# Kernel optimization log

Measured on AMD Instinct MI355X. Metric: run time of the kernel, lower is better.

## Reference

```python
import jax, jax.numpy as jnp
import numpy as np

EMBED_DIM = 1024
NUM_HEADS = 16
HEAD_DIM = EMBED_DIM // NUM_HEADS
VOCAB = 5          # languages
BOTTLENECK = 800
SCALING = HEAD_DIM ** -0.5


def setup_inputs() -> dict:
    key = jax.random.key(0)
    ks = jax.random.split(key, 16)
    T, B, D = 2048, 2, EMBED_DIM
    s = 0.02
    return {
        "query": jax.random.normal(ks[0], (T, B, D), jnp.float32),
        "key": jax.random.normal(ks[1], (T, B, D), jnp.float32),
        "value": jax.random.normal(ks[2], (T, B, D), jnp.float32),
        "wq": jax.random.normal(ks[3], (D, D), jnp.float32) * s,
        "bq": jnp.zeros((D,), jnp.float32),
        "wk": jax.random.normal(ks[4], (D, D), jnp.float32) * s,
        "bk": jnp.zeros((D,), jnp.float32),
        "wv": jax.random.normal(ks[5], (D, D), jnp.float32) * s,
        "bv": jnp.zeros((D,), jnp.float32),
        "wo": jax.random.normal(ks[6], (D, D), jnp.float32) * s,
        "bo": jnp.zeros((D,), jnp.float32),
        "wte": jax.random.normal(ks[7], (VOCAB, D), jnp.float32) * s,
        "ct_w1": jax.random.normal(ks[8], (VOCAB, BOTTLENECK, D), jnp.float32) * s,
        "ct_b1": jnp.zeros((VOCAB, BOTTLENECK), jnp.float32),
        "ct_w2": jax.random.normal(ks[9], (VOCAB, 2 * D, BOTTLENECK), jnp.float32) * s,
        "ct_b2": jnp.zeros((VOCAB, 2 * D), jnp.float32),
        "language_id": jax.random.randint(ks[10], (B,), 0, VOCAB, jnp.int32),
    }


def _prefix_kv(language_id, wte, ct_w1, ct_b1, ct_w2, ct_b2):
    # PrefixTuningLangEmbLangspec: embed lang id, run all 5 bottleneck MLPs,
    # select per-sample MLP output via one-hot weighting, split into K/V.
    B = language_id.shape[0]
    emb = wte[language_id]                                  # [B, D]
    h = jnp.tanh(jnp.einsum("bd,chd->cbh", emb, ct_w1) + ct_b1[:, None, :])  # [5,B,800]
    kv = jnp.einsum("cbh,cdh->cbd", h, ct_w2) + ct_b2[:, None, :]            # [5,B,2D]
    w = jax.nn.one_hot(language_id, VOCAB, dtype=kv.dtype)  # [B,5]
    kv_sel = jnp.einsum("bc,cbd->bd", w, kv)                # [B,2D]
    # view(b,1,2,nh,hd): first D -> keys, second D -> values
    pk = kv_sel[:, :EMBED_DIM].reshape(B, NUM_HEADS, 1, HEAD_DIM)
    pv = kv_sel[:, EMBED_DIM:].reshape(B, NUM_HEADS, 1, HEAD_DIM)
    return pk, pv


def reference(query, key, value, wq, bq, wk, bk, wv, bv, wo, bo,
              wte, ct_w1, ct_b1, ct_w2, ct_b2, language_id):
    T, B, D = query.shape
    pk, pv = _prefix_kv(language_id, wte, ct_w1, ct_b1, ct_w2, ct_b2)  # [B,H,1,hd]

    # separate Q/K/V projections (Linear: x @ W^T + b)
    q = (jnp.einsum("tbd,ed->tbe", query, wq) + bq) * SCALING
    k = jnp.einsum("tbd,ed->tbe", key, wk) + bk
    v = jnp.einsum("tbd,ed->tbe", value, wv) + bv

    # [T,B,D] -> [B,H,T,hd]
    def split_heads(x):
        return x.reshape(T, B, NUM_HEADS, HEAD_DIM).transpose(1, 2, 0, 3)

    qh = split_heads(q)
    kh = jnp.concatenate([pk, split_heads(k)], axis=2)  # [B,H,T+1,hd]
    vh = jnp.concatenate([pv, split_heads(v)], axis=2)

    scores = jnp.einsum("bhqd,bhkd->bhqk", qh, kh)      # [B,H,T,T+1]
    attn = jax.nn.softmax(scores, axis=-1)
    ctx = jnp.einsum("bhqk,bhkd->bhqd", attn, vh)       # [B,H,T,hd]

    ctx = ctx.transpose(2, 0, 1, 3).reshape(T, B, D)    # back to [T,B,D]
    out = jnp.einsum("tbd,ed->tbe", ctx, wo) + bo
    return out
```

## Files before the change

### kernel.cpp

```cpp
#include <hip/hip_runtime.h>
#include <stdint.h>

#define T_SEQ 2048
#define BATCH 2
#define DIM   1024
#define NH    16
#define HD    64
#define TKP   2112

typedef _Float16 v8h __attribute__((ext_vector_type(8)));
typedef _Float16 v4h __attribute__((ext_vector_type(4)));
typedef float    f32x4 __attribute__((ext_vector_type(4)));

__device__ __forceinline__ void gload16(const _Float16* g, _Float16* l) {
  __builtin_amdgcn_global_load_lds(
      (__attribute__((address_space(1))) unsigned int*)g,
      (__attribute__((address_space(3))) unsigned int*)l, 16, 0, 0);
}

__global__ void cvt_all(const float4* __restrict__ s0, const float4* __restrict__ s1,
                        const float4* __restrict__ s2, const float4* __restrict__ s3,
                        const float4* __restrict__ s4, const float4* __restrict__ s5,
                        const float4* __restrict__ s6,
                        v4h* __restrict__ d0, v4h* __restrict__ d1, v4h* __restrict__ d2,
                        v4h* __restrict__ d3, v4h* __restrict__ d4, v4h* __restrict__ d5,
                        v4h* __restrict__ d6) {
  const int NTB4 = 1048576, DD4 = 262144;
  int i = blockIdx.x * 256 + threadIdx.x;
  const float4* s; v4h* d; int off;
  if (i < 3 * NTB4) {
    int t = i / NTB4; off = i - t * NTB4;
    s = t == 0 ? s0 : t == 1 ? s1 : s2;
    d = t == 0 ? d0 : t == 1 ? d1 : d2;
  } else {
    int j = i - 3 * NTB4;
    int t = j / DD4; off = j - t * DD4;
    s = t == 0 ? s3 : t == 1 ? s4 : t == 2 ? s5 : s6;
    d = t == 0 ? d3 : t == 1 ? d4 : t == 2 ? d5 : d6;
  }
  float4 v = s[off];
  v4h o = { (_Float16)v.x, (_Float16)v.y, (_Float16)v.z, (_Float16)v.w };
  d[off] = o;
}

__global__ void prefix_h_k(const float* __restrict__ wte, const float* __restrict__ w1,
                           const float* __restrict__ b1, const int* __restrict__ lang,
                           float* __restrict__ hbuf) {
  int wid = blockIdx.x * 4 + (threadIdx.x >> 6);
  int lane = threadIdx.x & 63;
  int b = wid / 800, j = wid - b * 800;
  int c = lang[b];
  const float* wr = w1 + ((size_t)c * 800 + j) * 1024;
  const float* em = wte + (size_t)c * 1024;
  float s = 0.f;
  for (int d = lane; d < 1024; d += 64) s += wr[d] * em[d];
  for (int off = 32; off > 0; off >>= 1) s += __shfl_down(s, off, 64);
  if (lane == 0) hbuf[wid] = tanhf(s + b1[c * 800 + j]);
}

__global__ void prefix_kv_k(const float* __restrict__ w2, const float* __restrict__ b2,
                            const float* __restrict__ hbuf, const int* __restrict__ lang,
                            _Float16* __restrict__ kb, _Float16* __restrict__ vb) {
  int wid = blockIdx.x * 4 + (threadIdx.x >> 6);
  int lane = threadIdx.x & 63;
  int b = wid >> 11, e = wid & 2047;
  int c = lang[b];
  const float* wr = w2 + ((size_t)c * 2048 + e) * 800;
  const float* hb = hbuf + b * 800;
  float s = 0.f;
  for (int j = lane; j < 800; j += 64) s += wr[j] * hb[j];
  for (int off = 32; off > 0; off >>= 1) s += __shfl_down(s, off, 64);
  if (lane == 0) {
    float val = s + b2[c * 2048 + e];
    if (e < 1024) {
      int h = e >> 6, hd = e & 63;
      kb[((size_t)(b * 16 + h) * TKP + 2048) * 64 + hd] = (_Float16)val;
    } else {
      int d = e - 1024;
      int h = d >> 6, hd = d & 63;
      vb[((size_t)(b * 16 + h) * 64 + hd) * TKP + 2048] = (_Float16)val;
    }
  }
}

__global__ void pad_k(_Float16* kb, _Float16* vb) {
  int bh = blockIdx.x;
  v8h z = {};
  _Float16* kp = kb + ((size_t)bh * TKP + 2048) * 64;
  for (int i = threadIdx.x; i < 512; i += 256) *(v8h*)&kp[i * 8] = z;
  for (int i = threadIdx.x; i < 512; i += 256) {
    int c = i >> 3, seg = i & 7;
    *(v8h*)&vb[((size_t)bh * 64 + c) * TKP + 2048 + seg * 8] = z;
  }
}

__global__ __launch_bounds__(256) void gemm_bt_k(
    const _Float16* __restrict__ A0, const _Float16* __restrict__ A1, const _Float16* __restrict__ A2,
    const _Float16* __restrict__ W0, const _Float16* __restrict__ W1, const _Float16* __restrict__ W2,
    const float* __restrict__ bs0, const float* __restrict__ bs1, const float* __restrict__ bs2,
    _Float16* __restrict__ qb, _Float16* __restrict__ kb, _Float16* __restrict__ vb,
    float* __restrict__ fout, int mode_base)
{
  __shared__ __align__(16) _Float16 smem[128 * 64 * 2];
  _Float16* As = smem;
  _Float16* Bs = smem + 128 * 64;
  const int mode = mode_base + blockIdx.z;
  const _Float16* A = (mode == 1) ? A1 : (mode == 2) ? A2 : A0;
  const _Float16* W = (mode == 1) ? W1 : (mode == 2) ? W2 : W0;
  const float* bias = (mode == 1) ? bs1 : (mode == 2) ? bs2 : bs0;
  const int tid = threadIdx.x, w = tid >> 6, lane = tid & 63;
  const int quad = lane >> 4, l15 = lane & 15;
  const int r0 = blockIdx.x * 128, c0 = blockIdx.y * 128;
  const int wm = w >> 1, wn = w & 1;
  const int srow = lane >> 3, sseg = lane & 7;
  f32x4 acc[4][4] = {};
  for (int k0 = 0; k0 < 1024; k0 += 64) {
    for (int i = 0; i < 4; ++i) {
      int rowb = w * 32 + i * 8;
      gload16(A + (size_t)(r0 + rowb + srow) * 1024 + k0 + sseg * 8, &As[rowb * 64]);
      gload16(W + (size_t)(c0 + rowb + srow) * 1024 + k0 + sseg * 8, &Bs[rowb * 64]);
    }
    __syncthreads();
    for (int ks = 0; ks < 2; ++ks) {
      v8h af[4], bfr[4];
      for (int mt = 0; mt < 4; ++mt)
        af[mt] = *(const v8h*)&As[(wm * 64 + mt * 16 + l15) * 64 + ks * 32 + quad * 8];
      for (int nt = 0; nt < 4; ++nt)
        bfr[nt] = *(const v8h*)&Bs[(wn * 64 + nt * 16 + l15) * 64 + ks * 32 + quad * 8];
      for (int mt = 0; mt < 4; ++mt)
        for (int nt = 0; nt < 4; ++nt)
          acc[mt][nt] = __builtin_amdgcn_mfma_f32_16x16x32_f16(af[mt], bfr[nt], acc[mt][nt], 0, 0, 0);
    }
    __syncthreads();
  }
  if (mode == 3) {
    for (int nt = 0; nt < 4; ++nt) {
      int e = c0 + wn * 64 + nt * 16 + l15;
      float be = bias[e];
      for (int mt = 0; mt < 4; ++mt) {
        int rb = r0 + wm * 64 + mt * 16 + quad * 4;
        for (int reg = 0; reg < 4; ++reg)
          fout[(size_t)(rb + reg) * 1024 + e] = acc[mt][nt][reg] + be;
      }
    }
    return;
  }
  _Float16* st = smem + w * 4096;
  const float qscale = (mode == 0) ? 0.125f * 1.44269504088896341f : 1.0f;
  for (int p = 0; p < 2; ++p) {
    __syncthreads();
    for (int ntl = 0; ntl < 2; ++ntl) {
      int nt = p * 2 + ntl;
      int e = c0 + wn * 64 + nt * 16 + l15;
      float be = bias[e];
      for (int mt = 0; mt < 4; ++mt)
        for (int reg = 0; reg < 4; ++reg) {
          float val = (acc[mt][nt][reg] + be) * qscale;
          int rl = mt * 16 + quad * 4 + reg;
          if (mode != 2) st[rl * 40 + ntl * 16 + l15] = (_Float16)val;
          else st[(ntl * 16 + l15) * 72 + (rl & 1) * 32 + (rl >> 1)] = (_Float16)val;
        }
    }
    __syncthreads();
    if (mode != 2) {
      for (int it = 0; it < 4; ++it) {
        int chunk = it * 64 + lane;
        int rr = chunk >> 2, seg = chunk & 3;
        v8h val = *(const v8h*)&st[rr * 40 + seg * 8];
        int r = r0 + wm * 64 + rr, b = r & 1, t = r >> 1;
        int e0 = c0 + wn * 64 + p * 32 + seg * 8;
        int h = e0 >> 6, hd0 = e0 & 63;
        if (mode == 0) *(v8h*)&qb[((size_t)(b * 16 + h) * 2048 + t) * 64 + hd0] = val;
        else           *(v8h*)&kb[((size_t)(b * 16 + h) * TKP + t) * 64 + hd0] = val;
      }
    } else {
      for (int it = 0; it < 4; ++it) {
        int chunk = it * 64 + lane;
        int el = chunk >> 3, b = (chunk >> 2) & 1, qs = chunk & 3;
        v8h val = *(const v8h*)&st[el * 72 + b * 32 + qs * 8];
        int e = c0 + wn * 64 + p * 32 + el;
        int h = e >> 6, hd = e & 63;
        int t0 = ((r0 + wm * 64) >> 1) + qs * 8;
        *(v8h*)&vb[((size_t)(b * 16 + h) * 64 + hd) * TKP + t0] = val;
      }
    }
  }
}

__global__ __launch_bounds__(256) void attn_k(
    const _Float16* __restrict__ qb, const _Float16* __restrict__ kb,
    const _Float16* __restrict__ vb, _Float16* __restrict__ ctx)
{
  __shared__ __align__(16) _Float16 Ks[2][64 * 72];
  __shared__ __align__(16) _Float16 Vs[2][64 * 72];
  __shared__ __align__(16) _Float16 Ps[128 * 72];
  const int bh = blockIdx.x;
  const int qt0 = blockIdx.y * 128;
  const int tid = threadIdx.x, w = tid >> 6, lane = tid & 63;
  const int quad = lane >> 4, l15 = lane & 15;
  v8h qf[2][2];
  for (int nt = 0; nt < 2; ++nt)
    for (int ks = 0; ks < 2; ++ks)
      qf[nt][ks] = *(const v8h*)(qb + ((size_t)bh * 2048 + qt0 + w * 32 + nt * 16 + l15) * 64
                                 + ks * 32 + quad * 8);
  const int sr = tid >> 3, sseg = tid & 7;
  const _Float16* kptr = kb + (size_t)bh * TKP * 64 + sr * 64 + sseg * 8;
  const _Float16* vptr = vb + (size_t)bh * 64 * TKP + (size_t)sr * TKP + sseg * 8;
  int4 kp0 = *(const int4*)kptr, kp1 = *(const int4*)(kptr + 2048);
  int4 vp0 = *(const int4*)vptr, vp1 = *(const int4*)(vptr + 32 * TKP);
  kptr += 4096; vptr += 64;
  f32x4 O[4][2] = {};
  f32x4 lacc[2] = {};
  const v8h vones = { (_Float16)1.f, (_Float16)1.f, (_Float16)1.f, (_Float16)1.f,
                      (_Float16)1.f, (_Float16)1.f, (_Float16)1.f, (_Float16)1.f };
  for (int kc = 0; kc < 33; ++kc) {
    _Float16* Kb = Ks[kc & 1];
    _Float16* Vb = Vs[kc & 1];
    *(int4*)&Kb[sr * 72 + sseg * 8] = kp0;
    *(int4*)&Kb[(sr + 32) * 72 + sseg * 8] = kp1;
    *(int4*)&Vb[sr * 72 + sseg * 8] = vp0;
    *(int4*)&Vb[(sr + 32) * 72 + sseg * 8] = vp1;
    __syncthreads();
    if (kc < 32) {
      kp0 = *(const int4*)kptr; kp1 = *(const int4*)(kptr + 2048);
      vp0 = *(const int4*)vptr; vp1 = *(const int4*)(vptr + 32 * TKP);
      kptr += 4096; vptr += 64;
    }
    f32x4 S[4][2] = {};
    for (int ks = 0; ks < 2; ++ks) {
      for (int mt = 0; mt < 4; ++mt) {
        v8h ak = *(const v8h*)&Kb[(mt * 16 + l15) * 72 + ks * 32 + quad * 8];
        S[mt][0] = __builtin_amdgcn_mfma_f32_16x16x32_f16(ak, qf[0][ks], S[mt][0], 0, 0, 0);
        S[mt][1] = __builtin_amdgcn_mfma_f32_16x16x32_f16(ak, qf[1][ks], S[mt][1], 0, 0, 0);
      }
    }
    if (kc == 32) {
      for (int mt = 0; mt < 4; ++mt)
        for (int reg = 0; reg < 4; ++reg)
          if (mt * 16 + quad * 4 + reg > 0) { S[mt][0][reg] = -1e30f; S[mt][1][reg] = -1e30f; }
    }
    for (int nt = 0; nt < 2; ++nt)
      for (int mt = 0; mt < 4; ++mt) {
        v4h pk4 = { (_Float16)__builtin_amdgcn_exp2f(S[mt][nt][0]),
                    (_Float16)__builtin_amdgcn_exp2f(S[mt][nt][1]),
                    (_Float16)__builtin_amdgcn_exp2f(S[mt][nt][2]),
                    (_Float16)__builtin_amdgcn_exp2f(S[mt][nt][3]) };
        *(v4h*)&Ps[(w * 32 + nt * 16 + l15) * 72 + mt * 16 + quad * 4] = pk4;
      }
    for (int ks = 0; ks < 2; ++ks) {
      v8h p0 = *(const v8h*)&Ps[(w * 32 + l15) * 72 + ks * 32 + quad * 8];
      v8h p1 = *(const v8h*)&Ps[(w * 32 + 16 + l15) * 72 + ks * 32 + quad * 8];
      for (int ht = 0; ht < 4; ++ht) {
        v8h av = *(const v8h*)&Vb[(ht * 16 + l15) * 72 + ks * 32 + quad * 8];
        O[ht][0] = __builtin_amdgcn_mfma_f32_16x16x32_f16(av, p0, O[ht][0], 0, 0, 0);
        O[ht][1] = __builtin_amdgcn_mfma_f32_16x16x32_f16(av, p1, O[ht][1], 0, 0, 0);
      }
      lacc[0] = __builtin_amdgcn_mfma_f32_16x16x32_f16(vones, p0, lacc[0], 0, 0, 0);
      lacc[1] = __builtin_amdgcn_mfma_f32_16x16x32_f16(vones, p1, lacc[1], 0, 0, 0);
    }
  }
  const int b = bh >> 4, hh = bh & 15;
  for (int nt = 0; nt < 2; ++nt) {
    float inv = 1.f / lacc[nt][0];
    int q = qt0 + w * 32 + nt * 16 + l15;
    for (int ht = 0; ht < 4; ++ht) {
      v4h o4 = { (_Float16)(O[ht][nt][0] * inv), (_Float16)(O[ht][nt][1] * inv),
                 (_Float16)(O[ht][nt][2] * inv), (_Float16)(O[ht][nt][3] * inv) };
      *(v4h*)(ctx + ((size_t)q * 2 + b) * 1024 + hh * 64 + ht * 16 + quad * 4) = o4;
    }
  }
}

extern "C" void kernel_launch(void* const* d_in, const int* in_sizes, int n_in,
                              void* d_out, int out_size, void* d_ws, size_t ws_size,
                              hipStream_t stream) {
  (void)in_sizes; (void)n_in; (void)out_size; (void)ws_size;
  const float* query = (const float*)d_in[0];
  const float* key_  = (const float*)d_in[1];
  const float* value = (const float*)d_in[2];
  const float* wq = (const float*)d_in[3];
  const float* bq = (const float*)d_in[4];
  const float* wk = (const float*)d_in[5];
  const float* bk = (const float*)d_in[6];
  const float* wv = (const float*)d_in[7];
  const float* bv = (const float*)d_in[8];
  const float* wo = (const float*)d_in[9];
  const float* bo = (const float*)d_in[10];
  const float* wte = (const float*)d_in[11];
  const float* w1 = (const float*)d_in[12];
  const float* b1 = (const float*)d_in[13];
  const float* w2 = (const float*)d_in[14];
  const float* b2 = (const float*)d_in[15];
  const int* lang = (const int*)d_in[16];
  float* out = (float*)d_out;

  const size_t NTB = (size_t)T_SEQ * BATCH * DIM;
  const size_t DD  = (size_t)DIM * DIM;
  const size_t KVN = (size_t)BATCH * NH * TKP * HD;
  _Float16* xq  = (_Float16*)d_ws;
  _Float16* xk  = xq + NTB;
  _Float16* xv  = xk + NTB;
  _Float16* wqb = xv + NTB;
  _Float16* wkb = wqb + DD;
  _Float16* wvb = wkb + DD;
  _Float16* wob = wvb + DD;
  _Float16* qbuf = wob + DD;
  _Float16* kbuf = qbuf + NTB;
  _Float16* vbuf = kbuf + KVN;
  float* hbuf = (float*)(vbuf + KVN);
  _Float16* ctxb = xq;

  cvt_all<<<16384, 256, 0, stream>>>((const float4*)query, (const float4*)key_,
                                     (const float4*)value, (const float4*)wq,
                                     (const float4*)wk, (const float4*)wv, (const float4*)wo,
                                     (v4h*)xq, (v4h*)xk, (v4h*)xv, (v4h*)wqb,
                                     (v4h*)wkb, (v4h*)wvb, (v4h*)wob);
  pad_k<<<32, 256, 0, stream>>>(kbuf, vbuf);
  prefix_h_k<<<400, 256, 0, stream>>>(wte, w1, b1, lang, hbuf);
  prefix_kv_k<<<1024, 256, 0, stream>>>(w2, b2, hbuf, lang, kbuf, vbuf);
  gemm_bt_k<<<dim3(32, 8, 3), 256, 0, stream>>>(xq, xk, xv, wqb, wkb, wvb, bq, bk, bv,
                                                qbuf, kbuf, vbuf, nullptr, 0);
  attn_k<<<dim3(32, 16), 256, 0, stream>>>(qbuf, kbuf, vbuf, ctxb);
  gemm_bt_k<<<dim3(32, 8, 1), 256, 0, stream>>>(ctxb, ctxb, ctxb, wob, wob, wob, bo, bo, bo,
                                                qbuf, kbuf, vbuf, out, 3);
}
```

Baseline: 307.5 us.

## Use 32x32 MFMA in attention with register-resident P and fuse pad kernel

Rewrites the attention inner loop to use 32x32x16 MFMA tiles. The exponentiated scores now stay in registers and feed the PV product directly, which removes the shared-memory P round trip and the ones-vector MFMA that computed the row sum; the row sum is now a scalar reduction. V is stored into LDS with a permuted column layout so the P fragment lines up with the output fragment, and s_setprio hints are placed around the MFMA blocks. The separate pad kernel is folded into the prefix-h kernel to save one launch, at the cost of more intricate layout correctness.

```diff
diff --git a/kernel.cpp b/kernel.cpp
--- a/kernel.cpp
+++ b/kernel.cpp
@@ -11,6 +11,7 @@
 typedef _Float16 v8h __attribute__((ext_vector_type(8)));
 typedef _Float16 v4h __attribute__((ext_vector_type(4)));
 typedef float    f32x4 __attribute__((ext_vector_type(4)));
+typedef float    f32x16 __attribute__((ext_vector_type(16)));
 
 __device__ __forceinline__ void gload16(const _Float16* g, _Float16* l) {
   __builtin_amdgcn_global_load_lds(
@@ -43,9 +44,21 @@
   d[off] = o;
 }
 
-__global__ void prefix_h_k(const float* __restrict__ wte, const float* __restrict__ w1,
-                           const float* __restrict__ b1, const int* __restrict__ lang,
-                           float* __restrict__ hbuf) {
+__global__ void prefix_pad_k(const float* __restrict__ wte, const float* __restrict__ w1,
+                             const float* __restrict__ b1, const int* __restrict__ lang,
+                             float* __restrict__ hbuf,
+                             _Float16* __restrict__ kb, _Float16* __restrict__ vb) {
+  if (blockIdx.x >= 400) {
+    int bh = blockIdx.x - 400;
+    v8h z = {};
+    _Float16* kp = kb + ((size_t)bh * TKP + 2048) * 64;
+    for (int i = threadIdx.x; i < 512; i += 256) *(v8h*)&kp[i * 8] = z;
+    for (int i = threadIdx.x; i < 512; i += 256) {
+      int c = i >> 3, seg = i & 7;
+      *(v8h*)&vb[((size_t)bh * 64 + c) * TKP + 2048 + seg * 8] = z;
+    }
+    return;
+  }
   int wid = blockIdx.x * 4 + (threadIdx.x >> 6);
   int lane = threadIdx.x & 63;
   int b = wid / 800, j = wid - b * 800;
@@ -80,17 +93,6 @@
       int h = d >> 6, hd = d & 63;
       vb[((size_t)(b * 16 + h) * 64 + hd) * TKP + 2048] = (_Float16)val;
     }
-  }
-}
-
-__global__ void pad_k(_Float16* kb, _Float16* vb) {
-  int bh = blockIdx.x;
-  v8h z = {};
-  _Float16* kp = kb + ((size_t)bh * TKP + 2048) * 64;
-  for (int i = threadIdx.x; i < 512; i += 256) *(v8h*)&kp[i * 8] = z;
-  for (int i = threadIdx.x; i < 512; i += 256) {
-    int c = i >> 3, seg = i & 7;
-    *(v8h*)&vb[((size_t)bh * 64 + c) * TKP + 2048 + seg * 8] = z;
   }
 }
 
@@ -193,81 +195,98 @@
 {
   __shared__ __align__(16) _Float16 Ks[2][64 * 72];
   __shared__ __align__(16) _Float16 Vs[2][64 * 72];
-  __shared__ __align__(16) _Float16 Ps[128 * 72];
   const int bh = blockIdx.x;
   const int qt0 = blockIdx.y * 128;
   const int tid = threadIdx.x, w = tid >> 6, lane = tid & 63;
-  const int quad = lane >> 4, l15 = lane & 15;
-  v8h qf[2][2];
-  for (int nt = 0; nt < 2; ++nt)
-    for (int ks = 0; ks < 2; ++ks)
-      qf[nt][ks] = *(const v8h*)(qb + ((size_t)bh * 2048 + qt0 + w * 32 + nt * 16 + l15) * 64
-                                 + ks * 32 + quad * 8);
+  const int l31 = lane & 31, h8 = (lane >> 5) * 8;
+  v8h qf[4];
+#pragma unroll
+  for (int t = 0; t < 4; ++t)
+    qf[t] = *(const v8h*)(qb + ((size_t)bh * 2048 + qt0 + w * 32 + l31) * 64 + t * 16 + h8);
   const int sr = tid >> 3, sseg = tid & 7;
   const _Float16* kptr = kb + (size_t)bh * TKP * 64 + sr * 64 + sseg * 8;
   const _Float16* vptr = vb + (size_t)bh * 64 * TKP + (size_t)sr * TKP + sseg * 8;
   int4 kp0 = *(const int4*)kptr, kp1 = *(const int4*)(kptr + 2048);
   int4 vp0 = *(const int4*)vptr, vp1 = *(const int4*)(vptr + 32 * TKP);
   kptr += 4096; vptr += 64;
-  f32x4 O[4][2] = {};
-  f32x4 lacc[2] = {};
-  const v8h vones = { (_Float16)1.f, (_Float16)1.f, (_Float16)1.f, (_Float16)1.f,
-                      (_Float16)1.f, (_Float16)1.f, (_Float16)1.f, (_Float16)1.f };
+  const int vcb = (sseg >> 1) * 32 + (sseg & 1) * 8;
+  f32x16 O0 = {}, O1 = {};
+  float l_ = 0.f;
   for (int kc = 0; kc < 33; ++kc) {
     _Float16* Kb = Ks[kc & 1];
     _Float16* Vb = Vs[kc & 1];
     *(int4*)&Kb[sr * 72 + sseg * 8] = kp0;
     *(int4*)&Kb[(sr + 32) * 72 + sseg * 8] = kp1;
-    *(int4*)&Vb[sr * 72 + sseg * 8] = vp0;
-    *(int4*)&Vb[(sr + 32) * 72 + sseg * 8] = vp1;
+    {
+      char* vr0 = (char*)&Vb[sr * 72];
+      char* vr1 = (char*)&Vb[(sr + 32) * 72];
+      *(int2*)(vr0 + vcb)      = *(int2*)&vp0;
+      *(int2*)(vr0 + vcb + 16) = *((int2*)&vp0 + 1);
+      *(int2*)(vr1 + vcb)      = *(int2*)&vp1;
+      *(int2*)(vr1 + vcb + 16) = *((int2*)&vp1 + 1);
+    }
     __syncthreads();
     if (kc < 32) {
       kp0 = *(const int4*)kptr; kp1 = *(const int4*)(kptr + 2048);
       vp0 = *(const int4*)vptr; vp1 = *(const int4*)(vptr + 32 * TKP);
       kptr += 4096; vptr += 64;
     }
-    f32x4 S[4][2] = {};
-    for (int ks = 0; ks < 2; ++ks) {
-      for (int mt = 0; mt < 4; ++mt) {
-        v8h ak = *(const v8h*)&Kb[(mt * 16 + l15) * 72 + ks * 32 + quad * 8];
-        S[mt][0] = __builtin_amdgcn_mfma_f32_16x16x32_f16(ak, qf[0][ks], S[mt][0], 0, 0, 0);
-        S[mt][1] = __builtin_amdgcn_mfma_f32_16x16x32_f16(ak, qf[1][ks], S[mt][1], 0, 0, 0);
+    f32x16 S0 = {}, S1 = {};
+    __builtin_amdgcn_s_setprio(1);
+#pragma unroll
+    for (int t = 0; t < 4; ++t) {
+      v8h kf0 = *(const v8h*)&Kb[(l31) * 72 + t * 16 + h8];
+      v8h kf1 = *(const v8h*)&Kb[(32 + l31) * 72 + t * 16 + h8];
+      S0 = __builtin_amdgcn_mfma_f32_32x32x16_f16(kf0, qf[t], S0, 0, 0, 0);
+      S1 = __builtin_amdgcn_mfma_f32_32x32x16_f16(kf1, qf[t], S1, 0, 0, 0);
+    }
+    __builtin_amdgcn_s_setprio(0);
+    if (kc == 32) {
+#pragma unroll
+      for (int r = 0; r < 16; ++r) {
+        if (r > 0) S0[r] = -1e30f;
+        S1[r] = -1e30f;
       }
-    }
-    if (kc == 32) {
-      for (int mt = 0; mt < 4; ++mt)
-        for (int reg = 0; reg < 4; ++reg)
-          if (mt * 16 + quad * 4 + reg > 0) { S[mt][0][reg] = -1e30f; S[mt][1][reg] = -1e30f; }
-    }
-    for (int nt = 0; nt < 2; ++nt)
-      for (int mt = 0; mt < 4; ++mt) {
-        v4h pk4 = { (_Float16)__builtin_amdgcn_exp2f(S[mt][nt][0]),
-                    (_Float16)__builtin_amdgcn_exp2f(S[mt][nt][1]),
-                    (_Float16)__builtin_amdgcn_exp2f(S[mt][nt][2]),
-                    (_Float16)__builtin_amdgcn_exp2f(S[mt][nt][3]) };
-        *(v4h*)&Ps[(w * 32 + nt * 16 + l15) * 72 + mt * 16 + quad * 4] = pk4;
-      }
-    for (int ks = 0; ks < 2; ++ks) {
-      v8h p0 = *(const v8h*)&Ps[(w * 32 + l15) * 72 + ks * 32 + quad * 8];
-      v8h p1 = *(const v8h*)&Ps[(w * 32 + 16 + l15) * 72 + ks * 32 + quad * 8];
-      for (int ht = 0; ht < 4; ++ht) {
-        v8h av = *(const v8h*)&Vb[(ht * 16 + l15) * 72 + ks * 32 + quad * 8];
-        O[ht][0] = __builtin_amdgcn_mfma_f32_16x16x32_f16(av, p0, O[ht][0], 0, 0, 0);
-        O[ht][1] = __builtin_amdgcn_mfma_f32_16x16x32_f16(av, p1, O[ht][1], 0, 0, 0);
-      }
-      lacc[0] = __builtin_amdgcn_mfma_f32_16x16x32_f16(vones, p0, lacc[0], 0, 0, 0);
-      lacc[1] = __builtin_amdgcn_mfma_f32_16x16x32_f16(vones, p1, lacc[1], 0, 0, 0);
-    }
-  }
+      if (lane >= 32) S0[0] = -1e30f;
+    }
+    float rs = 0.f;
+#pragma unroll
+    for (int r = 0; r < 16; ++r) { S0[r] = __builtin_amdgcn_exp2f(S0[r]); rs += S0[r]; }
+#pragma unroll
+    for (int r = 0; r < 16; ++r) { S1[r] = __builtin_amdgcn_exp2f(S1[r]); rs += S1[r]; }
+    l_ += rs;
+    __builtin_amdgcn_s_setprio(1);
+#pragma unroll
+    for (int c = 0; c < 4; ++c) {
+      v8h ph;
+      if (c == 0)      ph = (v8h){ (_Float16)S0[0], (_Float16)S0[1], (_Float16)S0[2], (_Float16)S0[3],
+                                   (_Float16)S0[4], (_Float16)S0[5], (_Float16)S0[6], (_Float16)S0[7] };
+      else if (c == 1) ph = (v8h){ (_Float16)S0[8], (_Float16)S0[9], (_Float16)S0[10], (_Float16)S0[11],
+                                   (_Float16)S0[12], (_Float16)S0[13], (_Float16)S0[14], (_Float16)S0[15] };
+      else if (c == 2) ph = (v8h){ (_Float16)S1[0], (_Float16)S1[1], (_Float16)S1[2], (_Float16)S1[3],
+                                   (_Float16)S1[4], (_Float16)S1[5], (_Float16)S1[6], (_Float16)S1[7] };
+      else             ph = (v8h){ (_Float16)S1[8], (_Float16)S1[9], (_Float16)S1[10], (_Float16)S1[11],
+                                   (_Float16)S1[12], (_Float16)S1[13], (_Float16)S1[14], (_Float16)S1[15] };
+      v8h vf0 = *(const v8h*)&Vb[(l31) * 72 + c * 16 + h8];
+      v8h vf1 = *(const v8h*)&Vb[(32 + l31) * 72 + c * 16 + h8];
+      O0 = __builtin_amdgcn_mfma_f32_32x32x16_f16(vf0, ph, O0, 0, 0, 0);
+      O1 = __builtin_amdgcn_mfma_f32_32x32x16_f16(vf1, ph, O1, 0, 0, 0);
+    }
+    __builtin_amdgcn_s_setprio(0);
+  }
+  l_ += __shfl_xor(l_, 32, 64);
+  const float inv = 1.f / l_;
   const int b = bh >> 4, hh = bh & 15;
-  for (int nt = 0; nt < 2; ++nt) {
-    float inv = 1.f / lacc[nt][0];
-    int q = qt0 + w * 32 + nt * 16 + l15;
-    for (int ht = 0; ht < 4; ++ht) {
-      v4h o4 = { (_Float16)(O[ht][nt][0] * inv), (_Float16)(O[ht][nt][1] * inv),
-                 (_Float16)(O[ht][nt][2] * inv), (_Float16)(O[ht][nt][3] * inv) };
-      *(v4h*)(ctx + ((size_t)q * 2 + b) * 1024 + hh * 64 + ht * 16 + quad * 4) = o4;
-    }
+  const int q = qt0 + w * 32 + l31;
+  _Float16* cbase = ctx + ((size_t)q * 2 + b) * 1024 + hh * 64 + (h8 >> 1);
+#pragma unroll
+  for (int rq = 0; rq < 4; ++rq) {
+    v4h o0 = { (_Float16)(O0[rq * 4 + 0] * inv), (_Float16)(O0[rq * 4 + 1] * inv),
+               (_Float16)(O0[rq * 4 + 2] * inv), (_Float16)(O0[rq * 4 + 3] * inv) };
+    *(v4h*)(cbase + rq * 8) = o0;
+    v4h o1 = { (_Float16)(O1[rq * 4 + 0] * inv), (_Float16)(O1[rq * 4 + 1] * inv),
+               (_Float16)(O1[rq * 4 + 2] * inv), (_Float16)(O1[rq * 4 + 3] * inv) };
+    *(v4h*)(cbase + 32 + rq * 8) = o1;
   }
 }
 
@@ -315,8 +334,7 @@
                                      (const float4*)wk, (const float4*)wv, (const float4*)wo,
                                      (v4h*)xq, (v4h*)xk, (v4h*)xv, (v4h*)wqb,
                                      (v4h*)wkb, (v4h*)wvb, (v4h*)wob);
-  pad_k<<<32, 256, 0, stream>>>(kbuf, vbuf);
-  prefix_h_k<<<400, 256, 0, stream>>>(wte, w1, b1, lang, hbuf);
+  prefix_pad_k<<<432, 256, 0, stream>>>(wte, w1, b1, lang, hbuf, kbuf, vbuf);
   prefix_kv_k<<<1024, 256, 0, stream>>>(w2, b2, hbuf, lang, kbuf, vbuf);
   gemm_bt_k<<<dim3(32, 8, 3), 256, 0, stream>>>(xq, xk, xv, wqb, wkb, wvb, bq, bk, bv,
                                                 qbuf, kbuf, vbuf, nullptr, 0);
```

After: 298.0 us. -3.1%, faster.
